# Kernel tuning notes

Measured on AMD Instinct MI355X. Metric: run time of the kernel, lower is better.

## Reference

```python
import jax, jax.numpy as jnp
import numpy as np

B, N, DIM = 4, 1024, 768
H, GP = 12, 64
HD = DIM // H
SCALE = HD ** -0.5


def setup_inputs() -> dict:
    key = jax.random.key(0)
    ks = jax.random.split(key, 7)
    s = DIM ** -0.5
    return {
        "x": jax.random.normal(ks[0], (B, N, DIM), dtype=jnp.float32),
        "W_qkv": jax.random.normal(ks[1], (3 * DIM, DIM), dtype=jnp.float32) * s,
        "b_qkv": jnp.zeros((3 * DIM,), dtype=jnp.float32),
        "W_gp": jax.random.normal(ks[2], (GP, DIM), dtype=jnp.float32) * s,
        "alpha": jax.random.normal(ks[3], (1, H, 1, 1), dtype=jnp.float32),
        "W_proj": jax.random.normal(ks[4], (DIM, DIM), dtype=jnp.float32) * s,
        "b_proj": jnp.zeros((DIM,), dtype=jnp.float32),
    }


def reference(x, W_qkv, b_qkv, W_gp, alpha, W_proj, b_proj):
    b, n, c = x.shape
    # qkv projection, split into heads: [b, h, n, hd]
    qkv = x @ W_qkv.T + b_qkv
    q, k, v = jnp.split(qkv, 3, axis=-1)
    def to_heads(t):
        return t.reshape(b, n, H, HD).transpose(0, 2, 1, 3)
    q, k, v = to_heads(q), to_heads(k), to_heads(v)

    # raw attention scores [b, h, n, n]
    attn = jnp.einsum('bhnd,bhmd->bhnm', q, k) * SCALE

    # group similarity: gp weight viewed as [h, gp, hd]
    gp = W_gp.reshape(H, GP, HD)
    gw = jnp.einsum('bhnd,hmd->bhnm', v, gp)          # [b, h, n, gp]
    gw = jax.nn.gelu(gw, approximate=False)           # exact GELU (torch default)
    gw = jax.nn.softmax(gw, axis=-1)
    G = jnp.einsum('bhnm,bhkm->bhnk', gw, gw)         # [b, h, n, n]

    # gated combination
    attn = jax.nn.softmax(attn * G, axis=-1)
    a = jax.nn.sigmoid(alpha)                          # [1, h, 1, 1]
    A = (1.0 - a) * attn + a * G
    # column-sum renormalization (sum over query dim 2)
    A = A / (A.sum(axis=2, keepdims=True) + 1e-8)

    out = jnp.einsum('bhnm,bhmd->bhnd', A, v)
    out = out.transpose(0, 2, 1, 3).reshape(b, n, c)
    return out @ W_proj.T + b_proj
```

## Files before the change

kernel.cpp:

```cpp
#include <hip/hip_runtime.h>
#include <math.h>

namespace {

constexpr int kN   = 1024;
constexpr int kDim = 768;
constexpr int kH   = 12;
constexpr int kBH  = 48;
constexpr float kScale = 0.125f;

typedef __attribute__((ext_vector_type(8))) short short8;
typedef __attribute__((ext_vector_type(4))) short short4v;
typedef __attribute__((ext_vector_type(4))) float f32x4;

#define MFMA(a, b, c) __builtin_amdgcn_mfma_f32_16x16x32_bf16(a, b, c, 0, 0, 0)

__device__ __forceinline__ ushort f2bf(float f) {
  uint u = __builtin_bit_cast(uint, f);
  u += 0x7fffu + ((u >> 16) & 1u);
  return (ushort)(u >> 16);
}
__device__ __forceinline__ float bf2f(ushort h) {
  uint u = ((uint)h) << 16;
  return __builtin_bit_cast(float, u);
}
__device__ __forceinline__ void split8(const float* f, short8& hi, short8& lo) {
  #pragma unroll
  for (int i = 0; i < 8; i++) {
    const ushort h = f2bf(f[i]);
    hi[i] = (short)h;
    lo[i] = (short)f2bf(f[i] - bf2f(h));
  }
}

__device__ __forceinline__ void gl16(const short* g, short* l) {
  __builtin_amdgcn_global_load_lds(
      (const __attribute__((address_space(1))) void*)g,
      (__attribute__((address_space(3))) void*)l, 16, 0, 0);
}

__device__ __forceinline__ short8 frag(const short* t, int row, int chunk) {
  return *(const short8*)(t + row * 64 + ((chunk ^ (row & 7)) << 3));
}

template<int ROWS, int W>
__device__ __forceinline__ void stage_tile(short* dst, const short* src,
                                           int stride, int w, int l) {
  #pragma unroll
  for (int c = 0; c < ROWS / 8; c += W) {
    const int cc = c + w;
    const int row0 = cc << 3;
    const int row = row0 + (l >> 3);
    const int ch = (l & 7) ^ (row & 7);
    gl16(src + (size_t)row * stride + (ch << 3), dst + row0 * 64);
  }
}

__global__ __launch_bounds__(256) void k_split(const float* __restrict__ src,
                                               short* __restrict__ h,
                                               short* __restrict__ l) {
  const size_t i = ((size_t)blockIdx.x * 256 + threadIdx.x) * 4;
  const float4 f = *(const float4*)(src + i);
  const float ff[4] = {f.x, f.y, f.z, f.w};
  short4v hv, lv;
  #pragma unroll
  for (int j = 0; j < 4; j++) {
    const ushort u = f2bf(ff[j]);
    hv[j] = (short)u;
    lv[j] = (short)f2bf(ff[j] - bf2f(u));
  }
  *(short4v*)(h + i) = hv;
  *(short4v*)(l + i) = lv;
}

__global__ __launch_bounds__(512) void k_qkv(const short* __restrict__ xh,
                                             const short* __restrict__ xl,
                                             const short* __restrict__ wh,
                                             const short* __restrict__ wl,
                                             const float* __restrict__ bias,
                                             short* __restrict__ qh, short* __restrict__ ql,
                                             short* __restrict__ kh, short* __restrict__ kl,
                                             short* __restrict__ vh, short* __restrict__ vl) {
  __shared__ __align__(16) short sb[2][32768];
  const int bx = blockIdx.x, by = blockIdx.y;
  const int tid = threadIdx.x, w = tid >> 6, lane = tid & 63;
  const int wr = w >> 2, wc = w & 3;
  const short* Asrc_h = xh + (size_t)(by * 128) * kDim;
  const short* Asrc_l = xl + (size_t)(by * 128) * kDim;
  const short* Bsrc_h = wh + (size_t)(bx * 128) * kDim;
  const short* Bsrc_l = wl + (size_t)(bx * 128) * kDim;

  f32x4 acc[4][2] = {};
  {
    short* nb = sb[0];
    stage_tile<128, 8>(nb,          Asrc_h, kDim, w, lane);
    stage_tile<128, 8>(nb + 8192,   Asrc_l, kDim, w, lane);
    stage_tile<128, 8>(nb + 16384,  Bsrc_h, kDim, w, lane);
    stage_tile<128, 8>(nb + 24576,  Bsrc_l, kDim, w, lane);
  }
  int p = 0;
  #pragma unroll 1
  for (int t = 0; t < 12; ++t) {
    __syncthreads();
    if (t < 11) {
      const int k0 = (t + 1) * 64;
      short* nb = sb[p ^ 1];
      stage_tile<128, 8>(nb,         Asrc_h + k0, kDim, w, lane);
      stage_tile<128, 8>(nb + 8192,  Asrc_l + k0, kDim, w, lane);
      stage_tile<128, 8>(nb + 16384, Bsrc_h + k0, kDim, w, lane);
      stage_tile<128, 8>(nb + 24576, Bsrc_l + k0, kDim, w, lane);
    }
    const short* cb = sb[p];
    #pragma unroll
    for (int s = 0; s < 2; ++s) {
      const int ch = (s << 2) + (lane >> 4);
      short8 af[4], alf[4], bf_[2], blf[2];
      #pragma unroll
      for (int i = 0; i < 4; i++) {
        const int ar = wr * 64 + i * 16 + (lane & 15);
        af[i]  = frag(cb, ar, ch);
        alf[i] = frag(cb + 8192, ar, ch);
      }
      #pragma unroll
      for (int j = 0; j < 2; j++) {
        const int br = wc * 32 + j * 16 + (lane & 15);
        bf_[j] = frag(cb + 16384, br, ch);
        blf[j] = frag(cb + 24576, br, ch);
      }
      #pragma unroll
      for (int i = 0; i < 4; i++)
        #pragma unroll
        for (int j = 0; j < 2; j++) {
          acc[i][j] = MFMA(af[i], bf_[j], acc[i][j]);
          acc[i][j] = MFMA(af[i], blf[j], acc[i][j]);
          acc[i][j] = MFMA(alf[i], bf_[j], acc[i][j]);
        }
    }
    p ^= 1;
  }
  #pragma unroll
  for (int j = 0; j < 2; j++) {
    const int col = bx * 128 + wc * 32 + j * 16 + (lane & 15);
    const int part = col / 768;
    const int rem = col - part * 768;
    const int hh = rem >> 6, d = rem & 63;
    short* dh = (part == 0) ? qh : ((part == 1) ? kh : vh);
    short* dl = (part == 0) ? ql : ((part == 1) ? kl : vl);
    const float bv = bias[col];
    #pragma unroll
    for (int i = 0; i < 4; i++) {
      #pragma unroll
      for (int r = 0; r < 4; r++) {
        const int gr = by * 128 + wr * 64 + i * 16 + ((lane >> 4) << 2) + r;
        const int b = gr >> 10, n = gr & 1023;
        const float val = acc[i][j][r] + bv;
        const ushort hu = f2bf(val);
        const size_t idx = (size_t)((b * kH + hh) * kN + n) * 64 + d;
        dh[idx] = (short)hu;
        dl[idx] = (short)f2bf(val - bf2f(hu));
      }
    }
  }
}

__global__ __launch_bounds__(512) void k_gw(const short* __restrict__ vh,
                                            const short* __restrict__ vl,
                                            const float* __restrict__ Wgp,
                                            short* __restrict__ gwh,
                                            short* __restrict__ gwl) {
  const int bh = blockIdx.x;
  const int h = bh % kH;
  const int n0 = blockIdx.y << 7;
  const int tid = threadIdx.x, w = tid >> 6, lane = tid & 63;
  __shared__ __align__(16) short gph[4096], gpl[4096];
  {
    const int r = tid >> 3, c = tid & 7;
    float f[8] __attribute__((aligned(16)));
    *(float4*)(f + 0) = *(const float4*)(Wgp + h * 4096 + r * 64 + c * 8);
    *(float4*)(f + 4) = *(const float4*)(Wgp + h * 4096 + r * 64 + c * 8 + 4);
    short8 hh, ll;
    split8(f, hh, ll);
    const int slot = c ^ (r & 7);
    *(short8*)(gph + r * 64 + slot * 8) = hh;
    *(short8*)(gpl + r * 64 + slot * 8) = ll;
  }
  short8 vhf[2], vlf[2];
  const size_t arow = (size_t)(bh * kN + n0 + w * 16 + (lane & 15)) * 64 + ((lane >> 4) << 3);
  vhf[0] = *(const short8*)(vh + arow); vhf[1] = *(const short8*)(vh + arow + 32);
  vlf[0] = *(const short8*)(vl + arow); vlf[1] = *(const short8*)(vl + arow + 32);
  __syncthreads();

  f32x4 aU[4] = {};
  #pragma unroll
  for (int msub = 0; msub < 4; msub++) {
    #pragma unroll
    for (int s = 0; s < 2; s++) {
      const int row = (msub << 4) + (lane & 15);
      const int ch = (s << 2) + (lane >> 4);
      const short8 bh_ = frag(gph, row, ch);
      const short8 bl_ = frag(gpl, row, ch);
      aU[msub] = MFMA(vhf[s], bh_, aU[msub]);
      aU[msub] = MFMA(vhf[s], bl_, aU[msub]);
      aU[msub] = MFMA(vlf[s], bh_, aU[msub]);
    }
  }
  #pragma unroll
  for (int r = 0; r < 4; r++) {
    float u[4];
    #pragma unroll
    for (int m = 0; m < 4; m++) {
      const float a = aU[m][r];
      u[m] = 0.5f * a * (1.0f + erff(a * 0.70710678118654752f));
    }
    float mx = fmaxf(fmaxf(u[0], u[1]), fmaxf(u[2], u[3]));
    #pragma unroll
    for (int msk = 1; msk < 16; msk <<= 1) mx = fmaxf(mx, __shfl_xor(mx, msk));
    float e[4], ssum = 0.f;
    #pragma unroll
    for (int m = 0; m < 4; m++) { e[m] = __expf(u[m] - mx); ssum += e[m]; }
    #pragma unroll
    for (int msk = 1; msk < 16; msk <<= 1) ssum += __shfl_xor(ssum, msk);
    const float inv = 1.0f / ssum;
    const int n = n0 + w * 16 + ((lane >> 4) << 2) + r;
    #pragma unroll
    for (int m = 0; m < 4; m++) {
      const float g = e[m] * inv;
      const ushort hu = f2bf(g);
      const size_t idx = (size_t)(bh * kN + n) * 64 + (m << 4) + (lane & 15);
      gwh[idx] = (short)hu;
      gwl[idx] = (short)f2bf(g - bf2f(hu));
    }
  }
}

__global__ __launch_bounds__(256) void k_vt(const short* __restrict__ vh,
                                            short* __restrict__ vtg) {
  const int bh = blockIdx.x;
  const int n0 = blockIdx.y << 6;
  __shared__ short t[64][80];
  const int tid = threadIdx.x;
  {
    const int n = tid >> 2, d0 = (tid & 3) << 4;
    const short8 a = *(const short8*)(vh + (size_t)(bh * kN + n0 + n) * 64 + d0);
    const short8 b = *(const short8*)(vh + (size_t)(bh * kN + n0 + n) * 64 + d0 + 8);
    #pragma unroll
    for (int i = 0; i < 8; ++i) { t[d0 + i][n] = a[i]; t[d0 + 8 + i][n] = b[i]; }
  }
  __syncthreads();
  const int d = tid >> 2, j0 = (tid & 3) << 4;
  short* dst = vtg + (size_t)bh * 65536 + (size_t)d * 1024 + n0 + j0;
  *(short8*)(dst)     = *(const short8*)(&t[d][j0]);
  *(short8*)(dst + 8) = *(const short8*)(&t[d][j0 + 8]);
}

__global__ __launch_bounds__(512) void k_denom(const short* __restrict__ qh,
                                               const short* __restrict__ ql,
                                               const short* __restrict__ kh,
                                               const short* __restrict__ kl,
                                               const short* __restrict__ gwh,
                                               const short* __restrict__ gwl,
                                               float* __restrict__ rdenom) {
  const int bh = blockIdx.x;
  const int n0 = blockIdx.y << 7;
  const int tid = threadIdx.x, w = tid >> 6, lane = tid & 63;
  __shared__ __align__(16) short sb[2][16384];

  short8 qhf[2], qlf[2], ghf[2], glf[2];
  {
    const size_t arow = (size_t)(bh * kN + n0 + w * 16 + (lane & 15)) * 64 + ((lane >> 4) << 3);
    qhf[0] = *(const short8*)(qh + arow);  qhf[1] = *(const short8*)(qh + arow + 32);
    qlf[0] = *(const short8*)(ql + arow);  qlf[1] = *(const short8*)(ql + arow + 32);
    ghf[0] = *(const short8*)(gwh + arow); ghf[1] = *(const short8*)(gwh + arow + 32);
    glf[0] = *(const short8*)(gwl + arow); glf[1] = *(const short8*)(gwl + arow + 32);
  }
  {
    const size_t mo = (size_t)bh * kN * 64;
    short* nb = sb[0];
    stage_tile<64, 8>(nb,         kh + mo, 64, w, lane);
    stage_tile<64, 8>(nb + 4096,  kl + mo, 64, w, lane);
    stage_tile<64, 8>(nb + 8192,  gwh + mo, 64, w, lane);
    stage_tile<64, 8>(nb + 12288, gwl + mo, 64, w, lane);
  }
  float dsum[4] = {0.f, 0.f, 0.f, 0.f};
  int p = 0;
  #pragma unroll 1
  for (int t = 0; t < 16; ++t) {
    __syncthreads();
    if (t < 15) {
      const size_t mo = (size_t)(bh * kN + (t + 1) * 64) * 64;
      short* nb = sb[p ^ 1];
      stage_tile<64, 8>(nb,         kh + mo, 64, w, lane);
      stage_tile<64, 8>(nb + 4096,  kl + mo, 64, w, lane);
      stage_tile<64, 8>(nb + 8192,  gwh + mo, 64, w, lane);
      stage_tile<64, 8>(nb + 12288, gwl + mo, 64, w, lane);
    }
    const short* cb = sb[p];
    #pragma unroll
    for (int msub = 0; msub < 4; msub++) {
      f32x4 aS = {0.f, 0.f, 0.f, 0.f}, aG = {0.f, 0.f, 0.f, 0.f};
      #pragma unroll
      for (int s = 0; s < 2; s++) {
        const int row = (msub << 4) + (lane & 15);
        const int ch = (s << 2) + (lane >> 4);
        const short8 bh_ = frag(cb, row, ch);
        const short8 bl_ = frag(cb + 4096, row, ch);
        const short8 eh_ = frag(cb + 8192, row, ch);
        const short8 el_ = frag(cb + 12288, row, ch);
        aS = MFMA(qhf[s], bh_, aS); aG = MFMA(ghf[s], eh_, aG);
        aS = MFMA(qhf[s], bl_, aS); aG = MFMA(ghf[s], el_, aG);
        aS = MFMA(qlf[s], bh_, aS); aG = MFMA(glf[s], eh_, aG);
      }
      #pragma unroll
      for (int r = 0; r < 4; r++)
        dsum[r] += __expf(aS[r] * kScale * aG[r]);
    }
    p ^= 1;
  }
  #pragma unroll
  for (int r = 0; r < 4; r++) {
    #pragma unroll
    for (int msk = 1; msk < 16; msk <<= 1)
      dsum[r] += __shfl_xor(dsum[r], msk);
  }
  if ((lane & 15) == 0) {
    #pragma unroll
    for (int r = 0; r < 4; r++)
      rdenom[bh * kN + n0 + w * 16 + ((lane >> 4) << 2) + r] = 1.0f / dsum[r];
  }
}

__global__ __launch_bounds__(512) void k_colsum(const short* __restrict__ qh,
                                                const short* __restrict__ ql,
                                                const short* __restrict__ kh,
                                                const short* __restrict__ kl,
                                                const short* __restrict__ gwh,
                                                const short* __restrict__ gwl,
                                                const float* __restrict__ rdenom,
                                                const float* __restrict__ alpha,
                                                float* __restrict__ rcolv) {
  const int bh = blockIdx.x;
  const int m0b = blockIdx.y << 7;
  const int tid = threadIdx.x, w = tid >> 6, lane = tid & 63;
  __shared__ __align__(16) short sb[2][16384];
  const float ah_ = 1.0f / (1.0f + __expf(-alpha[bh % kH]));
  const float om = 1.0f - ah_;

  short8 khf[2], klf[2], ghf[2], glf[2];
  {
    const size_t arow = (size_t)(bh * kN + m0b + w * 16 + (lane & 15)) * 64 + ((lane >> 4) << 3);
    khf[0] = *(const short8*)(kh + arow);  khf[1] = *(const short8*)(kh + arow + 32);
    klf[0] = *(const short8*)(kl + arow);  klf[1] = *(const short8*)(kl + arow + 32);
    ghf[0] = *(const short8*)(gwh + arow); ghf[1] = *(const short8*)(gwh + arow + 32);
    glf[0] = *(const short8*)(gwl + arow); glf[1] = *(const short8*)(gwl + arow + 32);
  }
  {
    const size_t no = (size_t)bh * kN * 64;
    short* nb = sb[0];
    stage_tile<64, 8>(nb,         qh + no, 64, w, lane);
    stage_tile<64, 8>(nb + 4096,  ql + no, 64, w, lane);
    stage_tile<64, 8>(nb + 8192,  gwh + no, 64, w, lane);
    stage_tile<64, 8>(nb + 12288, gwl + no, 64, w, lane);
  }
  float csum[4] = {0.f, 0.f, 0.f, 0.f};
  int p = 0;
  #pragma unroll 1
  for (int t = 0; t < 16; ++t) {
    __syncthreads();
    if (t < 15) {
      const size_t no = (size_t)(bh * kN + (t + 1) * 64) * 64;
      short* nb = sb[p ^ 1];
      stage_tile<64, 8>(nb,         qh + no, 64, w, lane);
      stage_tile<64, 8>(nb + 4096,  ql + no, 64, w, lane);
      stage_tile<64, 8>(nb + 8192,  gwh + no, 64, w, lane);
      stage_tile<64, 8>(nb + 12288, gwl + no, 64, w, lane);
    }
    const short* cb = sb[p];
    #pragma unroll
    for (int nsub = 0; nsub < 4; nsub++) {
      f32x4 aS = {0.f, 0.f, 0.f, 0.f}, aG = {0.f, 0.f, 0.f, 0.f};
      #pragma unroll
      for (int s = 0; s < 2; s++) {
        const int row = (nsub << 4) + (lane & 15);
        const int ch = (s << 2) + (lane >> 4);
        const short8 bh_ = frag(cb, row, ch);
        const short8 bl_ = frag(cb + 4096, row, ch);
        const short8 eh_ = frag(cb + 8192, row, ch);
        const short8 el_ = frag(cb + 12288, row, ch);
        aS = MFMA(khf[s], bh_, aS); aG = MFMA(ghf[s], eh_, aG);
        aS = MFMA(khf[s], bl_, aS); aG = MFMA(ghf[s], el_, aG);
        aS = MFMA(klf[s], bh_, aS); aG = MFMA(glf[s], eh_, aG);
      }
      const float rd = rdenom[bh * kN + t * 64 + (nsub << 4) + (lane & 15)];
      #pragma unroll
      for (int r = 0; r < 4; r++) {
        const float g = aG[r];
        csum[r] += om * (__expf(aS[r] * kScale * g) * rd) + ah_ * g;
      }
    }
    p ^= 1;
  }
  #pragma unroll
  for (int r = 0; r < 4; r++) {
    #pragma unroll
    for (int msk = 1; msk < 16; msk <<= 1)
      csum[r] += __shfl_xor(csum[r], msk);
  }
  if ((lane & 15) == 0) {
    #pragma unroll
    for (int r = 0; r < 4; r++)
      rcolv[bh * kN + m0b + w * 16 + ((lane >> 4) << 2) + r] = 1.0f / (csum[r] + 1e-8f);
  }
}

__global__ __launch_bounds__(512) void k_out(const short* __restrict__ qh,
                                             const short* __restrict__ ql,
                                             const short* __restrict__ kh,
                                             const short* __restrict__ kl,
                                             const short* __restrict__ vtg,
                                             const short* __restrict__ gwh,
                                             const short* __restrict__ gwl,
                                             const float* __restrict__ rdenom,
                                             const float* __restrict__ rcolv,
                                             const float* __restrict__ alpha,
                                             short* __restrict__ ctxh,
                                             short* __restrict__ ctxl) {
  const int bh = blockIdx.x;
  const int h = bh % kH;
  const int b = bh / kH;
  const int n0 = blockIdx.y << 7;
  const int tid = threadIdx.x, w = tid >> 6, lane = tid & 63;
  __shared__ __align__(16) short sb[2][20480];
  __shared__ __align__(16) short pls[8192];
  const float ah_ = 1.0f / (1.0f + __expf(-alpha[h]));
  const float om = 1.0f - ah_;

  short8 qhf[2], qlf[2], ghf[2], glf[2];
  float rdn[4];
  {
    const size_t arow = (size_t)(bh * kN + n0 + w * 16 + (lane & 15)) * 64 + ((lane >> 4) << 3);
    qhf[0] = *(const short8*)(qh + arow);  qhf[1] = *(const short8*)(qh + arow + 32);
    qlf[0] = *(const short8*)(ql + arow);  qlf[1] = *(const short8*)(ql + arow + 32);
    ghf[0] = *(const short8*)(gwh + arow); ghf[1] = *(const short8*)(gwh + arow + 32);
    glf[0] = *(const short8*)(gwl + arow); glf[1] = *(const short8*)(gwl + arow + 32);
    #pragma unroll
    for (int r = 0; r < 4; r++)
      rdn[r] = rdenom[bh * kN + n0 + w * 16 + ((lane >> 4) << 2) + r];
  }
  {
    const size_t mo = (size_t)bh * kN * 64;
    short* nb = sb[0];
    stage_tile<64, 8>(nb,         kh + mo, 64, w, lane);
    stage_tile<64, 8>(nb + 4096,  kl + mo, 64, w, lane);
    stage_tile<64, 8>(nb + 8192,  gwh + mo, 64, w, lane);
    stage_tile<64, 8>(nb + 12288, gwl + mo, 64, w, lane);
    stage_tile<64, 8>(nb + 16384, vtg + (size_t)bh * 65536, kN, w, lane);
  }
  f32x4 oac[4] = {{0.f,0.f,0.f,0.f},{0.f,0.f,0.f,0.f},{0.f,0.f,0.f,0.f},{0.f,0.f,0.f,0.f}};
  short* pw = pls + w * 1024;
  int p = 0;
  #pragma unroll 1
  for (int t = 0; t < 16; ++t) {
    __syncthreads();
    if (t < 15) {
      const size_t mo = (size_t)(bh * kN + (t + 1) * 64) * 64;
      short* nb = sb[p ^ 1];
      stage_tile<64, 8>(nb,         kh + mo, 64, w, lane);
      stage_tile<64, 8>(nb + 4096,  kl + mo, 64, w, lane);
      stage_tile<64, 8>(nb + 8192,  gwh + mo, 64, w, lane);
      stage_tile<64, 8>(nb + 12288, gwl + mo, 64, w, lane);
      stage_tile<64, 8>(nb + 16384, vtg + (size_t)bh * 65536 + (t + 1) * 64, kN, w, lane);
    }
    const short* cb = sb[p];
    #pragma unroll
    for (int msub = 0; msub < 4; msub++) {
      f32x4 aS = {0.f, 0.f, 0.f, 0.f}, aG = {0.f, 0.f, 0.f, 0.f};
      #pragma unroll
      for (int s = 0; s < 2; s++) {
        const int row = (msub << 4) + (lane & 15);
        const int ch = (s << 2) + (lane >> 4);
        const short8 bh_ = frag(cb, row, ch);
        const short8 bl_ = frag(cb + 4096, row, ch);
        const short8 eh_ = frag(cb + 8192, row, ch);
        const short8 el_ = frag(cb + 12288, row, ch);
        aS = MFMA(qhf[s], bh_, aS); aG = MFMA(ghf[s], eh_, aG);
        aS = MFMA(qhf[s], bl_, aS); aG = MFMA(ghf[s], el_, aG);
        aS = MFMA(qlf[s], bh_, aS); aG = MFMA(glf[s], eh_, aG);
      }
      const float rc = rcolv[bh * kN + t * 64 + (msub << 4) + (lane & 15)];
      #pragma unroll
      for (int r = 0; r < 4; r++) {
        const float g = aG[r];
        const float pp = __expf(aS[r] * kScale * g) * rdn[r];
        const float a = (om * pp + ah_ * g) * rc;
        const int prow = ((lane >> 4) << 2) + r;
        const int pcol = (msub << 4) + (lane & 15);
        pw[prow * 64 + (((pcol >> 3) ^ (prow & 7)) << 3) + (pcol & 7)] = (short)f2bf(a);
      }
    }
    #pragma unroll
    for (int s = 0; s < 2; s++) {
      const short8 pa = frag(pw, lane & 15, (s << 2) + (lane >> 4));
      #pragma unroll
      for (int dsub = 0; dsub < 4; dsub++) {
        const short8 vb_ = frag(cb + 16384, (dsub << 4) + (lane & 15), (s << 2) + (lane >> 4));
        oac[dsub] = MFMA(pa, vb_, oac[dsub]);
      }
    }
    p ^= 1;
  }
  #pragma unroll
  for (int dsub = 0; dsub < 4; dsub++) {
    #pragma unroll
    for (int r = 0; r < 4; r++) {
      const int n = n0 + w * 16 + ((lane >> 4) << 2) + r;
      const int d = (dsub << 4) + (lane & 15);
      const float val = oac[dsub][r];
      const ushort hu = f2bf(val);
      const size_t idx = (size_t)(b * kN + n) * kDim + h * 64 + d;
      ctxh[idx] = (short)hu;
      ctxl[idx] = (short)f2bf(val - bf2f(hu));
    }
  }
}

__global__ __launch_bounds__(512) void k_proj(const short* __restrict__ ch_,
                                              const short* __restrict__ cl_,
                                              const short* __restrict__ wh,
                                              const short* __restrict__ wl,
                                              const float* __restrict__ bias,
                                              float* __restrict__ out) {
  __shared__ __align__(16) short sb[2][32768];
  const int bx = blockIdx.x, by = blockIdx.y;
  const int tid = threadIdx.x, w = tid >> 6, lane = tid & 63;
  const int wr = w >> 2, wc = w & 3;
  const short* Asrc_h = ch_ + (size_t)(by * 128) * kDim;
  const short* Asrc_l = cl_ + (size_t)(by * 128) * kDim;
  const short* Bsrc_h = wh + (size_t)(bx * 128) * kDim;
  const short* Bsrc_l = wl + (size_t)(bx * 128) * kDim;

  f32x4 acc[4][2] = {};
  {
    short* nb = sb[0];
    stage_tile<128, 8>(nb,         Asrc_h, kDim, w, lane);
    stage_tile<128, 8>(nb + 8192,  Asrc_l, kDim, w, lane);
    stage_tile<128, 8>(nb + 16384, Bsrc_h, kDim, w, lane);
    stage_tile<128, 8>(nb + 24576, Bsrc_l, kDim, w, lane);
  }
  int p = 0;
  #pragma unroll 1
  for (int t = 0; t < 12; ++t) {
    __syncthreads();
    if (t < 11) {
      const int k0 = (t + 1) * 64;
      short* nb = sb[p ^ 1];
      stage_tile<128, 8>(nb,         Asrc_h + k0, kDim, w, lane);
      stage_tile<128, 8>(nb + 8192,  Asrc_l + k0, kDim, w, lane);
      stage_tile<128, 8>(nb + 16384, Bsrc_h + k0, kDim, w, lane);
      stage_tile<128, 8>(nb + 24576, Bsrc_l + k0, kDim, w, lane);
    }
    const short* cb = sb[p];
    #pragma unroll
    for (int s = 0; s < 2; ++s) {
      const int ch = (s << 2) + (lane >> 4);
      short8 af[4], alf[4], bf_[2], blf[2];
      #pragma unroll
      for (int i = 0; i < 4; i++) {
        const int ar = wr * 64 + i * 16 + (lane & 15);
        af[i]  = frag(cb, ar, ch);
        alf[i] = frag(cb + 8192, ar, ch);
      }
      #pragma unroll
      for (int j = 0; j < 2; j++) {
        const int br = wc * 32 + j * 16 + (lane & 15);
        bf_[j] = frag(cb + 16384, br, ch);
        blf[j] = frag(cb + 24576, br, ch);
      }
      #pragma unroll
      for (int i = 0; i < 4; i++)
        #pragma unroll
        for (int j = 0; j < 2; j++) {
          acc[i][j] = MFMA(af[i], bf_[j], acc[i][j]);
          acc[i][j] = MFMA(af[i], blf[j], acc[i][j]);
          acc[i][j] = MFMA(alf[i], bf_[j], acc[i][j]);
          acc[i][j] = MFMA(alf[i], blf[j], acc[i][j]);
        }
    }
    p ^= 1;
  }
  #pragma unroll
  for (int j = 0; j < 2; j++) {
    const int col = bx * 128 + wc * 32 + j * 16 + (lane & 15);
    const float bv = bias[col];
    #pragma unroll
    for (int i = 0; i < 4; i++) {
      #pragma unroll
      for (int r = 0; r < 4; r++) {
        const int row = by * 128 + wr * 64 + i * 16 + ((lane >> 4) << 2) + r;
        out[(size_t)row * kDim + col] = acc[i][j][r] + bv;
      }
    }
  }
}

}

extern "C" void kernel_launch(void* const* d_in, const int* in_sizes, int n_in,
                              void* d_out, int out_size, void* d_ws, size_t ws_size,
                              hipStream_t stream) {
  const float* x     = (const float*)d_in[0];
  const float* Wqkv  = (const float*)d_in[1];
  const float* bqkv  = (const float*)d_in[2];
  const float* Wgp   = (const float*)d_in[3];
  const float* alpha = (const float*)d_in[4];
  const float* Wproj = (const float*)d_in[5];
  const float* bproj = (const float*)d_in[6];
  float* out = (float*)d_out;

  const size_t he = 3145728;
  short* qh  = (short*)d_ws;
  short* ql  = qh + he;
  short* kh  = ql + he;
  short* kl  = kh + he;
  short* vh  = kl + he;
  short* vl  = vh + he;
  short* gwh = vl + he;
  short* gwl = gwh + he;
  short* xh  = gwl + he;
  short* xl  = xh + he;
  float* rdenom = (float*)(xl + he);
  float* rcolv  = rdenom + (size_t)kBH * kN;

  short* Wqh = gwh;  short* Wql = gwl;
  short* vtg = vl;
  short* ctxh = xh;  short* ctxl = xl;
  short* Wph = qh;   short* Wpl = ql;

  k_split<<<3072, 256, 0, stream>>>(x, xh, xl);
  k_split<<<1728, 256, 0, stream>>>(Wqkv, Wqh, Wql);
  k_qkv  <<<dim3(18, 32), 512, 0, stream>>>(xh, xl, Wqh, Wql, bqkv,
                                            qh, ql, kh, kl, vh, vl);
  k_gw   <<<dim3(kBH, 8), 512, 0, stream>>>(vh, vl, Wgp, gwh, gwl);
  k_vt   <<<dim3(kBH, 16), 256, 0, stream>>>(vh, vtg);
  k_denom<<<dim3(kBH, 8), 512, 0, stream>>>(qh, ql, kh, kl, gwh, gwl, rdenom);
  k_colsum<<<dim3(kBH, 8), 512, 0, stream>>>(qh, ql, kh, kl, gwh, gwl,
                                             rdenom, alpha, rcolv);
  k_out  <<<dim3(kBH, 8), 512, 0, stream>>>(qh, ql, kh, kl, vtg, gwh, gwl,
                                            rdenom, rcolv, alpha, ctxh, ctxl);
  k_split<<<576, 256, 0, stream>>>(Wproj, Wph, Wpl);
  k_proj <<<dim3(6, 32), 512, 0, stream>>>(ctxh, ctxl, Wph, Wpl, bproj, out);
}
```

Before: 271.9 us.

## Switch attention kernels to 32x32 MFMA and fold column norm into V

The denom, colsum and out kernels move from 16x16x32 to 32x32x16 bf16 MFMA tiles with 4 waves of 32 rows each. Single-buffered LDS staging replaces the double buffer. The column renormalization factor is now applied to V during the transpose kernel, which runs after colsum, so k_out no longer multiplies by it per element. The P tile is built in registers via lane shuffles instead of an LDS round trip, and the output is written through LDS for coalesced stores. Dropping the double buffer loses load/compute overlap, and rounding V*rc to bf16 changes numerics slightly.

```diff
diff --git a/kernel.cpp b/kernel.cpp
--- a/kernel.cpp
+++ b/kernel.cpp
@@ -12,8 +12,11 @@
 typedef __attribute__((ext_vector_type(8))) short short8;
 typedef __attribute__((ext_vector_type(4))) short short4v;
 typedef __attribute__((ext_vector_type(4))) float f32x4;
-
-#define MFMA(a, b, c) __builtin_amdgcn_mfma_f32_16x16x32_bf16(a, b, c, 0, 0, 0)
+typedef __attribute__((ext_vector_type(16))) float f32x16;
+typedef __attribute__((ext_vector_type(4))) uint uint4v;
+
+#define MFMA(a, b, c)   __builtin_amdgcn_mfma_f32_16x16x32_bf16(a, b, c, 0, 0, 0)
+#define MFMA32(a, b, c) __builtin_amdgcn_mfma_f32_32x32x16_bf16(a, b, c, 0, 0, 0)
 
 __device__ __forceinline__ ushort f2bf(float f) {
   uint u = __builtin_bit_cast(uint, f);
@@ -31,6 +34,9 @@
     hi[i] = (short)h;
     lo[i] = (short)f2bf(f[i] - bf2f(h));
   }
+}
+__device__ __forceinline__ uint packbf(float a, float b) {
+  return (uint)f2bf(a) | ((uint)f2bf(b) << 16);
 }
 
 __device__ __forceinline__ void gl16(const short* g, short* l) {
@@ -234,6 +240,7 @@
 }
 
 __global__ __launch_bounds__(256) void k_vt(const short* __restrict__ vh,
+                                            const float* __restrict__ rcolv,
                                             short* __restrict__ vtg) {
   const int bh = blockIdx.x;
   const int n0 = blockIdx.y << 6;
@@ -241,10 +248,14 @@
   const int tid = threadIdx.x;
   {
     const int n = tid >> 2, d0 = (tid & 3) << 4;
+    const float rc = rcolv[bh * kN + n0 + n];
     const short8 a = *(const short8*)(vh + (size_t)(bh * kN + n0 + n) * 64 + d0);
     const short8 b = *(const short8*)(vh + (size_t)(bh * kN + n0 + n) * 64 + d0 + 8);
     #pragma unroll
-    for (int i = 0; i < 8; ++i) { t[d0 + i][n] = a[i]; t[d0 + 8 + i][n] = b[i]; }
+    for (int i = 0; i < 8; ++i) {
+      t[d0 + i][n]     = (short)f2bf(bf2f((ushort)a[i]) * rc);
+      t[d0 + 8 + i][n] = (short)f2bf(bf2f((ushort)b[i]) * rc);
+    }
   }
   __syncthreads();
   const int d = tid >> 2, j0 = (tid & 3) << 4;
@@ -253,7 +264,7 @@
   *(short8*)(dst + 8) = *(const short8*)(&t[d][j0 + 8]);
 }
 
-__global__ __launch_bounds__(512) void k_denom(const short* __restrict__ qh,
+__global__ __launch_bounds__(256) void k_denom(const short* __restrict__ qh,
                                                const short* __restrict__ ql,
                                                const short* __restrict__ kh,
                                                const short* __restrict__ kl,
@@ -263,73 +274,59 @@
   const int bh = blockIdx.x;
   const int n0 = blockIdx.y << 7;
   const int tid = threadIdx.x, w = tid >> 6, lane = tid & 63;
-  __shared__ __align__(16) short sb[2][16384];
-
-  short8 qhf[2], qlf[2], ghf[2], glf[2];
-  {
-    const size_t arow = (size_t)(bh * kN + n0 + w * 16 + (lane & 15)) * 64 + ((lane >> 4) << 3);
-    qhf[0] = *(const short8*)(qh + arow);  qhf[1] = *(const short8*)(qh + arow + 32);
-    qlf[0] = *(const short8*)(ql + arow);  qlf[1] = *(const short8*)(ql + arow + 32);
-    ghf[0] = *(const short8*)(gwh + arow); ghf[1] = *(const short8*)(gwh + arow + 32);
-    glf[0] = *(const short8*)(gwl + arow); glf[1] = *(const short8*)(gwl + arow + 32);
-  }
-  {
-    const size_t mo = (size_t)bh * kN * 64;
-    short* nb = sb[0];
-    stage_tile<64, 8>(nb,         kh + mo, 64, w, lane);
-    stage_tile<64, 8>(nb + 4096,  kl + mo, 64, w, lane);
-    stage_tile<64, 8>(nb + 8192,  gwh + mo, 64, w, lane);
-    stage_tile<64, 8>(nb + 12288, gwl + mo, 64, w, lane);
-  }
-  float dsum[4] = {0.f, 0.f, 0.f, 0.f};
-  int p = 0;
+  const int lc = lane & 31, hl = lane >> 5;
+  __shared__ __align__(16) short sb[16384];
+
+  short8 qB[4], qlB[4], gB[4], glB[4];
+  {
+    const size_t nrow = (size_t)(bh * kN + n0 + w * 32 + lc) * 64;
+    #pragma unroll
+    for (int ks = 0; ks < 4; ks++) {
+      const int off = ks * 16 + (hl << 3);
+      qB[ks]  = *(const short8*)(qh  + nrow + off);
+      qlB[ks] = *(const short8*)(ql  + nrow + off);
+      gB[ks]  = *(const short8*)(gwh + nrow + off);
+      glB[ks] = *(const short8*)(gwl + nrow + off);
+    }
+  }
+  float dsum = 0.f;
   #pragma unroll 1
   for (int t = 0; t < 16; ++t) {
     __syncthreads();
-    if (t < 15) {
-      const size_t mo = (size_t)(bh * kN + (t + 1) * 64) * 64;
-      short* nb = sb[p ^ 1];
-      stage_tile<64, 8>(nb,         kh + mo, 64, w, lane);
-      stage_tile<64, 8>(nb + 4096,  kl + mo, 64, w, lane);
-      stage_tile<64, 8>(nb + 8192,  gwh + mo, 64, w, lane);
-      stage_tile<64, 8>(nb + 12288, gwl + mo, 64, w, lane);
-    }
-    const short* cb = sb[p];
-    #pragma unroll
-    for (int msub = 0; msub < 4; msub++) {
-      f32x4 aS = {0.f, 0.f, 0.f, 0.f}, aG = {0.f, 0.f, 0.f, 0.f};
-      #pragma unroll
-      for (int s = 0; s < 2; s++) {
-        const int row = (msub << 4) + (lane & 15);
-        const int ch = (s << 2) + (lane >> 4);
-        const short8 bh_ = frag(cb, row, ch);
-        const short8 bl_ = frag(cb + 4096, row, ch);
-        const short8 eh_ = frag(cb + 8192, row, ch);
-        const short8 el_ = frag(cb + 12288, row, ch);
-        aS = MFMA(qhf[s], bh_, aS); aG = MFMA(ghf[s], eh_, aG);
-        aS = MFMA(qhf[s], bl_, aS); aG = MFMA(ghf[s], el_, aG);
-        aS = MFMA(qlf[s], bh_, aS); aG = MFMA(glf[s], eh_, aG);
-      }
-      #pragma unroll
-      for (int r = 0; r < 4; r++)
-        dsum[r] += __expf(aS[r] * kScale * aG[r]);
-    }
-    p ^= 1;
-  }
-  #pragma unroll
-  for (int r = 0; r < 4; r++) {
-    #pragma unroll
-    for (int msk = 1; msk < 16; msk <<= 1)
-      dsum[r] += __shfl_xor(dsum[r], msk);
-  }
-  if ((lane & 15) == 0) {
-    #pragma unroll
-    for (int r = 0; r < 4; r++)
-      rdenom[bh * kN + n0 + w * 16 + ((lane >> 4) << 2) + r] = 1.0f / dsum[r];
-  }
-}
-
-__global__ __launch_bounds__(512) void k_colsum(const short* __restrict__ qh,
+    const size_t mo = (size_t)(bh * kN + t * 64) * 64;
+    stage_tile<64, 4>(sb,         kh  + mo, 64, w, lane);
+    stage_tile<64, 4>(sb + 4096,  kl  + mo, 64, w, lane);
+    stage_tile<64, 4>(sb + 8192,  gwh + mo, 64, w, lane);
+    stage_tile<64, 4>(sb + 12288, gwl + mo, 64, w, lane);
+    __syncthreads();
+    #pragma unroll
+    for (int at = 0; at < 2; ++at) {
+      f32x16 aS = {}, aG = {};
+      #pragma unroll
+      for (int ks = 0; ks < 4; ++ks) {
+        const int row = at * 32 + lc;
+        const int ck = ks * 2 + hl;
+        const short8 Ah_ = frag(sb, row, ck);
+        const short8 Al_ = frag(sb + 4096, row, ck);
+        const short8 Eh_ = frag(sb + 8192, row, ck);
+        const short8 El_ = frag(sb + 12288, row, ck);
+        aS = MFMA32(Ah_, qB[ks], aS);
+        aS = MFMA32(Al_, qB[ks], aS);
+        aS = MFMA32(Ah_, qlB[ks], aS);
+        aG = MFMA32(Eh_, gB[ks], aG);
+        aG = MFMA32(El_, gB[ks], aG);
+        aG = MFMA32(Eh_, glB[ks], aG);
+      }
+      #pragma unroll
+      for (int r = 0; r < 16; ++r)
+        dsum += __expf(aS[r] * kScale * aG[r]);
+    }
+  }
+  dsum += __shfl_xor(dsum, 32);
+  if (lane < 32) rdenom[bh * kN + n0 + w * 32 + lane] = 1.0f / dsum;
+}
+
+__global__ __launch_bounds__(256) void k_colsum(const short* __restrict__ qh,
                                                 const short* __restrict__ ql,
                                                 const short* __restrict__ kh,
                                                 const short* __restrict__ kl,
@@ -339,80 +336,68 @@
                                                 const float* __restrict__ alpha,
                                                 float* __restrict__ rcolv) {
   const int bh = blockIdx.x;
-  const int m0b = blockIdx.y << 7;
+  const int m0 = blockIdx.y << 7;
   const int tid = threadIdx.x, w = tid >> 6, lane = tid & 63;
-  __shared__ __align__(16) short sb[2][16384];
+  const int lc = lane & 31, hl = lane >> 5;
+  __shared__ __align__(16) short sb[16384];
+  __shared__ float rdl[64];
   const float ah_ = 1.0f / (1.0f + __expf(-alpha[bh % kH]));
   const float om = 1.0f - ah_;
 
-  short8 khf[2], klf[2], ghf[2], glf[2];
-  {
-    const size_t arow = (size_t)(bh * kN + m0b + w * 16 + (lane & 15)) * 64 + ((lane >> 4) << 3);
-    khf[0] = *(const short8*)(kh + arow);  khf[1] = *(const short8*)(kh + arow + 32);
-    klf[0] = *(const short8*)(kl + arow);  klf[1] = *(const short8*)(kl + arow + 32);
-    ghf[0] = *(const short8*)(gwh + arow); ghf[1] = *(const short8*)(gwh + arow + 32);
-    glf[0] = *(const short8*)(gwl + arow); glf[1] = *(const short8*)(gwl + arow + 32);
-  }
-  {
-    const size_t no = (size_t)bh * kN * 64;
-    short* nb = sb[0];
-    stage_tile<64, 8>(nb,         qh + no, 64, w, lane);
-    stage_tile<64, 8>(nb + 4096,  ql + no, 64, w, lane);
-    stage_tile<64, 8>(nb + 8192,  gwh + no, 64, w, lane);
-    stage_tile<64, 8>(nb + 12288, gwl + no, 64, w, lane);
-  }
-  float csum[4] = {0.f, 0.f, 0.f, 0.f};
-  int p = 0;
+  short8 kB[4], klB[4], gB[4], glB[4];
+  {
+    const size_t mrow = (size_t)(bh * kN + m0 + w * 32 + lc) * 64;
+    #pragma unroll
+    for (int ks = 0; ks < 4; ks++) {
+      const int off = ks * 16 + (hl << 3);
+      kB[ks]  = *(const short8*)(kh  + mrow + off);
+      klB[ks] = *(const short8*)(kl  + mrow + off);
+      gB[ks]  = *(const short8*)(gwh + mrow + off);
+      glB[ks] = *(const short8*)(gwl + mrow + off);
+    }
+  }
+  float csum = 0.f;
   #pragma unroll 1
   for (int t = 0; t < 16; ++t) {
     __syncthreads();
-    if (t < 15) {
-      const size_t no = (size_t)(bh * kN + (t + 1) * 64) * 64;
-      short* nb = sb[p ^ 1];
-      stage_tile<64, 8>(nb,         qh + no, 64, w, lane);
-      stage_tile<64, 8>(nb + 4096,  ql + no, 64, w, lane);
-      stage_tile<64, 8>(nb + 8192,  gwh + no, 64, w, lane);
-      stage_tile<64, 8>(nb + 12288, gwl + no, 64, w, lane);
-    }
-    const short* cb = sb[p];
-    #pragma unroll
-    for (int nsub = 0; nsub < 4; nsub++) {
-      f32x4 aS = {0.f, 0.f, 0.f, 0.f}, aG = {0.f, 0.f, 0.f, 0.f};
-      #pragma unroll
-      for (int s = 0; s < 2; s++) {
-        const int row = (nsub << 4) + (lane & 15);
-        const int ch = (s << 2) + (lane >> 4);
-        const short8 bh_ = frag(cb, row, ch);
-        const short8 bl_ = frag(cb + 4096, row, ch);
-        const short8 eh_ = frag(cb + 8192, row, ch);
-        const short8 el_ = frag(cb + 12288, row, ch);
-        aS = MFMA(khf[s], bh_, aS); aG = MFMA(ghf[s], eh_, aG);
-        aS = MFMA(khf[s], bl_, aS); aG = MFMA(ghf[s], el_, aG);
-        aS = MFMA(klf[s], bh_, aS); aG = MFMA(glf[s], eh_, aG);
-      }
-      const float rd = rdenom[bh * kN + t * 64 + (nsub << 4) + (lane & 15)];
-      #pragma unroll
-      for (int r = 0; r < 4; r++) {
+    const size_t no = (size_t)(bh * kN + t * 64) * 64;
+    stage_tile<64, 4>(sb,         qh  + no, 64, w, lane);
+    stage_tile<64, 4>(sb + 4096,  ql  + no, 64, w, lane);
+    stage_tile<64, 4>(sb + 8192,  gwh + no, 64, w, lane);
+    stage_tile<64, 4>(sb + 12288, gwl + no, 64, w, lane);
+    if (tid < 64) rdl[tid] = rdenom[bh * kN + t * 64 + tid];
+    __syncthreads();
+    #pragma unroll
+    for (int at = 0; at < 2; ++at) {
+      f32x16 aS = {}, aG = {};
+      #pragma unroll
+      for (int ks = 0; ks < 4; ++ks) {
+        const int row = at * 32 + lc;
+        const int ck = ks * 2 + hl;
+        const short8 Ah_ = frag(sb, row, ck);
+        const short8 Al_ = frag(sb + 4096, row, ck);
+        const short8 Eh_ = frag(sb + 8192, row, ck);
+        const short8 El_ = frag(sb + 12288, row, ck);
+        aS = MFMA32(Ah_, kB[ks], aS);
+        aS = MFMA32(Al_, kB[ks], aS);
+        aS = MFMA32(Ah_, klB[ks], aS);
+        aG = MFMA32(Eh_, gB[ks], aG);
+        aG = MFMA32(El_, gB[ks], aG);
+        aG = MFMA32(Eh_, glB[ks], aG);
+      }
+      #pragma unroll
+      for (int r = 0; r < 16; ++r) {
+        const int nr = at * 32 + (r & 3) + ((r >> 2) << 3) + (hl << 2);
         const float g = aG[r];
-        csum[r] += om * (__expf(aS[r] * kScale * g) * rd) + ah_ * g;
-      }
-    }
-    p ^= 1;
-  }
-  #pragma unroll
-  for (int r = 0; r < 4; r++) {
-    #pragma unroll
-    for (int msk = 1; msk < 16; msk <<= 1)
-      csum[r] += __shfl_xor(csum[r], msk);
-  }
-  if ((lane & 15) == 0) {
-    #pragma unroll
-    for (int r = 0; r < 4; r++)
-      rcolv[bh * kN + m0b + w * 16 + ((lane >> 4) << 2) + r] = 1.0f / (csum[r] + 1e-8f);
-  }
-}
-
-__global__ __launch_bounds__(512) void k_out(const short* __restrict__ qh,
+        csum += om * (__expf(aS[r] * kScale * g) * rdl[nr]) + ah_ * g;
+      }
+    }
+  }
+  csum += __shfl_xor(csum, 32);
+  if (lane < 32) rcolv[bh * kN + m0 + w * 32 + lane] = 1.0f / (csum + 1e-8f);
+}
+
+__global__ __launch_bounds__(256) void k_out(const short* __restrict__ qh,
                                              const short* __restrict__ ql,
                                              const short* __restrict__ kh,
                                              const short* __restrict__ kl,
@@ -420,7 +405,6 @@
                                              const short* __restrict__ gwh,
                                              const short* __restrict__ gwl,
                                              const float* __restrict__ rdenom,
-                                             const float* __restrict__ rcolv,
                                              const float* __restrict__ alpha,
                                              short* __restrict__ ctxh,
                                              short* __restrict__ ctxl) {
@@ -429,96 +413,112 @@
   const int b = bh / kH;
   const int n0 = blockIdx.y << 7;
   const int tid = threadIdx.x, w = tid >> 6, lane = tid & 63;
-  __shared__ __align__(16) short sb[2][20480];
-  __shared__ __align__(16) short pls[8192];
+  const int lc = lane & 31, hl = lane >> 5;
+  __shared__ __align__(16) short sb[20480];
   const float ah_ = 1.0f / (1.0f + __expf(-alpha[h]));
   const float om = 1.0f - ah_;
 
-  short8 qhf[2], qlf[2], ghf[2], glf[2];
-  float rdn[4];
-  {
-    const size_t arow = (size_t)(bh * kN + n0 + w * 16 + (lane & 15)) * 64 + ((lane >> 4) << 3);
-    qhf[0] = *(const short8*)(qh + arow);  qhf[1] = *(const short8*)(qh + arow + 32);
-    qlf[0] = *(const short8*)(ql + arow);  qlf[1] = *(const short8*)(ql + arow + 32);
-    ghf[0] = *(const short8*)(gwh + arow); ghf[1] = *(const short8*)(gwh + arow + 32);
-    glf[0] = *(const short8*)(gwl + arow); glf[1] = *(const short8*)(gwl + arow + 32);
-    #pragma unroll
-    for (int r = 0; r < 4; r++)
-      rdn[r] = rdenom[bh * kN + n0 + w * 16 + ((lane >> 4) << 2) + r];
-  }
-  {
-    const size_t mo = (size_t)bh * kN * 64;
-    short* nb = sb[0];
-    stage_tile<64, 8>(nb,         kh + mo, 64, w, lane);
-    stage_tile<64, 8>(nb + 4096,  kl + mo, 64, w, lane);
-    stage_tile<64, 8>(nb + 8192,  gwh + mo, 64, w, lane);
-    stage_tile<64, 8>(nb + 12288, gwl + mo, 64, w, lane);
-    stage_tile<64, 8>(nb + 16384, vtg + (size_t)bh * 65536, kN, w, lane);
-  }
-  f32x4 oac[4] = {{0.f,0.f,0.f,0.f},{0.f,0.f,0.f,0.f},{0.f,0.f,0.f,0.f},{0.f,0.f,0.f,0.f}};
-  short* pw = pls + w * 1024;
-  int p = 0;
+  short8 qB[4], qlB[4], gB[4], glB[4];
+  {
+    const size_t nrow = (size_t)(bh * kN + n0 + w * 32 + lc) * 64;
+    #pragma unroll
+    for (int ks = 0; ks < 4; ks++) {
+      const int off = ks * 16 + (hl << 3);
+      qB[ks]  = *(const short8*)(qh  + nrow + off);
+      qlB[ks] = *(const short8*)(ql  + nrow + off);
+      gB[ks]  = *(const short8*)(gwh + nrow + off);
+      glB[ks] = *(const short8*)(gwl + nrow + off);
+    }
+  }
+  const float rdn = rdenom[bh * kN + n0 + w * 32 + lc];
+  f32x16 oac[2] = {};
+
   #pragma unroll 1
   for (int t = 0; t < 16; ++t) {
     __syncthreads();
-    if (t < 15) {
-      const size_t mo = (size_t)(bh * kN + (t + 1) * 64) * 64;
-      short* nb = sb[p ^ 1];
-      stage_tile<64, 8>(nb,         kh + mo, 64, w, lane);
-      stage_tile<64, 8>(nb + 4096,  kl + mo, 64, w, lane);
-      stage_tile<64, 8>(nb + 8192,  gwh + mo, 64, w, lane);
-      stage_tile<64, 8>(nb + 12288, gwl + mo, 64, w, lane);
-      stage_tile<64, 8>(nb + 16384, vtg + (size_t)bh * 65536 + (t + 1) * 64, kN, w, lane);
-    }
-    const short* cb = sb[p];
-    #pragma unroll
-    for (int msub = 0; msub < 4; msub++) {
-      f32x4 aS = {0.f, 0.f, 0.f, 0.f}, aG = {0.f, 0.f, 0.f, 0.f};
-      #pragma unroll
-      for (int s = 0; s < 2; s++) {
-        const int row = (msub << 4) + (lane & 15);
-        const int ch = (s << 2) + (lane >> 4);
-        const short8 bh_ = frag(cb, row, ch);
-        const short8 bl_ = frag(cb + 4096, row, ch);
-        const short8 eh_ = frag(cb + 8192, row, ch);
-        const short8 el_ = frag(cb + 12288, row, ch);
-        aS = MFMA(qhf[s], bh_, aS); aG = MFMA(ghf[s], eh_, aG);
-        aS = MFMA(qhf[s], bl_, aS); aG = MFMA(ghf[s], el_, aG);
-        aS = MFMA(qlf[s], bh_, aS); aG = MFMA(glf[s], eh_, aG);
-      }
-      const float rc = rcolv[bh * kN + t * 64 + (msub << 4) + (lane & 15)];
-      #pragma unroll
-      for (int r = 0; r < 4; r++) {
+    const size_t mo = (size_t)(bh * kN + t * 64) * 64;
+    stage_tile<64, 4>(sb,         kh  + mo, 64, w, lane);
+    stage_tile<64, 4>(sb + 4096,  kl  + mo, 64, w, lane);
+    stage_tile<64, 4>(sb + 8192,  gwh + mo, 64, w, lane);
+    stage_tile<64, 4>(sb + 12288, gwl + mo, 64, w, lane);
+    stage_tile<64, 4>(sb + 16384, vtg + (size_t)bh * 65536 + t * 64, kN, w, lane);
+    __syncthreads();
+    short8 pf[4];
+    #pragma unroll
+    for (int at = 0; at < 2; ++at) {
+      f32x16 aS = {}, aG = {};
+      #pragma unroll
+      for (int ks = 0; ks < 4; ++ks) {
+        const int row = at * 32 + lc;
+        const int ck = ks * 2 + hl;
+        const short8 Ah_ = frag(sb, row, ck);
+        const short8 Al_ = frag(sb + 4096, row, ck);
+        const short8 Eh_ = frag(sb + 8192, row, ck);
+        const short8 El_ = frag(sb + 12288, row, ck);
+        aS = MFMA32(Ah_, qB[ks], aS);
+        aS = MFMA32(Al_, qB[ks], aS);
+        aS = MFMA32(Ah_, qlB[ks], aS);
+        aG = MFMA32(Eh_, gB[ks], aG);
+        aG = MFMA32(El_, gB[ks], aG);
+        aG = MFMA32(Eh_, glB[ks], aG);
+      }
+      float a[16];
+      #pragma unroll
+      for (int r = 0; r < 16; ++r) {
         const float g = aG[r];
-        const float pp = __expf(aS[r] * kScale * g) * rdn[r];
-        const float a = (om * pp + ah_ * g) * rc;
-        const int prow = ((lane >> 4) << 2) + r;
-        const int pcol = (msub << 4) + (lane & 15);
-        pw[prow * 64 + (((pcol >> 3) ^ (prow & 7)) << 3) + (pcol & 7)] = (short)f2bf(a);
-      }
-    }
-    #pragma unroll
-    for (int s = 0; s < 2; s++) {
-      const short8 pa = frag(pw, lane & 15, (s << 2) + (lane >> 4));
-      #pragma unroll
-      for (int dsub = 0; dsub < 4; dsub++) {
-        const short8 vb_ = frag(cb + 16384, (dsub << 4) + (lane & 15), (s << 2) + (lane >> 4));
-        oac[dsub] = MFMA(pa, vb_, oac[dsub]);
-      }
-    }
-    p ^= 1;
-  }
-  #pragma unroll
-  for (int dsub = 0; dsub < 4; dsub++) {
-    #pragma unroll
-    for (int r = 0; r < 4; r++) {
-      const int n = n0 + w * 16 + ((lane >> 4) << 2) + r;
-      const int d = (dsub << 4) + (lane & 15);
-      const float val = oac[dsub][r];
-      const ushort hu = f2bf(val);
-      const size_t idx = (size_t)(b * kN + n) * kDim + h * 64 + d;
-      ctxh[idx] = (short)hu;
-      ctxl[idx] = (short)f2bf(val - bf2f(hu));
+        const float p = __expf(aS[r] * kScale * g) * rdn;
+        a[r] = om * p + ah_ * g;
+      }
+      uint W[8], Ws[8];
+      #pragma unroll
+      for (int j = 0; j < 8; ++j) W[j] = packbf(a[2 * j], a[2 * j + 1]);
+      #pragma unroll
+      for (int j = 0; j < 8; ++j) Ws[j] = __shfl_xor(W[j], 32);
+      {
+        uint4v b0, b1;
+        b0[0] = hl ? Ws[2] : W[0];  b0[1] = hl ? Ws[3] : W[1];
+        b0[2] = hl ? W[2]  : Ws[0]; b0[3] = hl ? W[3]  : Ws[1];
+        b1[0] = hl ? Ws[6] : W[4];  b1[1] = hl ? Ws[7] : W[5];
+        b1[2] = hl ? W[6]  : Ws[4]; b1[3] = hl ? W[7]  : Ws[5];
+        pf[at * 2 + 0] = __builtin_bit_cast(short8, b0);
+        pf[at * 2 + 1] = __builtin_bit_cast(short8, b1);
+      }
+    }
+    #pragma unroll
+    for (int dt = 0; dt < 2; ++dt)
+      #pragma unroll
+      for (int ks = 0; ks < 4; ++ks) {
+        const short8 va = frag(sb + 16384, dt * 32 + lc, ks * 2 + hl);
+        oac[dt] = MFMA32(va, pf[ks], oac[dt]);
+      }
+  }
+  __syncthreads();
+  float* ow = (float*)sb;
+  const int wbase = w * 32 * 68;
+  #pragma unroll
+  for (int dt = 0; dt < 2; ++dt)
+    #pragma unroll
+    for (int r = 0; r < 16; ++r) {
+      const int d = dt * 32 + (r & 3) + ((r >> 2) << 3) + (hl << 2);
+      ow[wbase + lc * 68 + d] = oac[dt][r];
+    }
+  __syncthreads();
+  {
+    const int rowi = tid >> 1;
+    const int d0 = (tid & 1) << 5;
+    const float* src = ow + (rowi >> 5) * 32 * 68 + (rowi & 31) * 68 + d0;
+    float f[32] __attribute__((aligned(16)));
+    #pragma unroll
+    for (int j = 0; j < 8; ++j) *(float4*)(f + 4 * j) = *(const float4*)(src + 4 * j);
+    const int n = n0 + rowi;
+    short* dsth = ctxh + (size_t)(b * kN + n) * kDim + h * 64 + d0;
+    short* dstl = ctxl + (size_t)(b * kN + n) * kDim + h * 64 + d0;
+    #pragma unroll
+    for (int g8 = 0; g8 < 4; ++g8) {
+      short8 hi, lo;
+      split8(f + 8 * g8, hi, lo);
+      *(short8*)(dsth + 8 * g8) = hi;
+      *(short8*)(dstl + 8 * g8) = lo;
     }
   }
 }
@@ -640,12 +640,12 @@
   k_qkv  <<<dim3(18, 32), 512, 0, stream>>>(xh, xl, Wqh, Wql, bqkv,
                                             qh, ql, kh, kl, vh, vl);
   k_gw   <<<dim3(kBH, 8), 512, 0, stream>>>(vh, vl, Wgp, gwh, gwl);
-  k_vt   <<<dim3(kBH, 16), 256, 0, stream>>>(vh, vtg);
-  k_denom<<<dim3(kBH, 8), 512, 0, stream>>>(qh, ql, kh, kl, gwh, gwl, rdenom);
-  k_colsum<<<dim3(kBH, 8), 512, 0, stream>>>(qh, ql, kh, kl, gwh, gwl,
+  k_denom<<<dim3(kBH, 8), 256, 0, stream>>>(qh, ql, kh, kl, gwh, gwl, rdenom);
+  k_colsum<<<dim3(kBH, 8), 256, 0, stream>>>(qh, ql, kh, kl, gwh, gwl,
                                              rdenom, alpha, rcolv);
-  k_out  <<<dim3(kBH, 8), 512, 0, stream>>>(qh, ql, kh, kl, vtg, gwh, gwl,
-                                            rdenom, rcolv, alpha, ctxh, ctxl);
+  k_vt   <<<dim3(kBH, 16), 256, 0, stream>>>(vh, rcolv, vtg);
+  k_out  <<<dim3(kBH, 8), 256, 0, stream>>>(qh, ql, kh, kl, vtg, gwh, gwl,
+                                            rdenom, alpha, ctxh, ctxl);
   k_split<<<576, 256, 0, stream>>>(Wproj, Wph, Wpl);
   k_proj <<<dim3(6, 32), 512, 0, stream>>>(ctxh, ctxl, Wph, Wpl, bproj, out);
 }
```

After: 274.2 us. No clear change (+0.8%).
